# Kernel optimization log

Hardware: AMD Instinct MI355X
Metric: run time of the kernel (lower is better)

The kernel has to match this reference:

```python
import jax, jax.numpy as jnp
import numpy as np
from jax import lax

DISCOUNT = 0.99
NORMALIZE = True
EPS = 1e-9


def setup_inputs() -> dict:
    key = jax.random.key(0)
    k1, k2 = jax.random.split(key)
    B, T = 4096, 8192
    rewards = jax.random.normal(k1, (B, T), dtype=jnp.float32)
    done_flags = (jax.random.uniform(k2, (B, T)) < 0.01).astype(jnp.float32)
    return {"rewards": rewards, "done_flags": done_flags}


def _episode_returns(rewards, done_flags):
    # reverse-time recurrence: r_t = rew_t + gamma * r_{t+1} * (1 - done_t)
    rw = jnp.moveaxis(rewards, -1, 0)      # [T, B]
    dn = jnp.moveaxis(done_flags, -1, 0)   # [T, B]

    def step(carry, xs):
        r, d = xs
        ret = r + DISCOUNT * carry * (1.0 - d)
        return ret, ret

    # init carry = 0 makes the last step reduce to returns[-1] = rewards[-1]
    _, rets = lax.scan(step, jnp.zeros_like(rw[0]), (rw, dn), reverse=True)
    returns = jnp.moveaxis(rets, 0, -1)    # [B, T]

    if NORMALIZE:
        # torch: (returns - returns.mean()) / (returns.std(dim=-1) + 1e-9)
        # global mean, per-trajectory std (unbiased, matching torch default)
        std = jnp.std(returns, axis=-1, ddof=1, keepdims=True)
        returns = (returns - jnp.mean(returns)) / (std + EPS)
    return returns


def reference(rewards, done_flags):
    return _episode_returns(rewards, done_flags)
```

## Files before the change

kernel.cpp:

```cpp
#include <hip/hip_runtime.h>
#include <math.h>

#define TLEN   8192
#define BROWS  4096
#define NT     256
#define WPB    (NT / 64)
#define GRID   (BROWS / WPB)
#define TPW    256
#define NTW    (TLEN / TPW)
#define GAMMA  0.99f
#define EPSN   1e-9

typedef float f4 __attribute__((ext_vector_type(4)));

__device__ __forceinline__ void scan_tile4(const f4 r, const f4 d,
                                           const int lane, float& tc,
                                           float* __restrict__ dst,
                                           double& accS, double& accQ) {
  float rv[4], cv[4];
  rv[0] = r.x; rv[1] = r.y; rv[2] = r.z; rv[3] = r.w;
  cv[0] = fmaf(-GAMMA, d.x, GAMMA);
  cv[1] = fmaf(-GAMMA, d.y, GAMMA);
  cv[2] = fmaf(-GAMMA, d.z, GAMMA);
  cv[3] = fmaf(-GAMMA, d.w, GAMMA);

  float A = 0.f, P = 1.f;
#pragma unroll
  for (int j = 3; j >= 0; --j) {
    A = fmaf(cv[j], A, rv[j]);
    P *= cv[j];
    rv[j] = A;
    cv[j] = P;
  }

  float sA = A, sP = P;
#pragma unroll
  for (int dd = 1; dd < 64; dd <<= 1) {
    const float tA = __shfl_down(sA, dd);
    const float tP = __shfl_down(sP, dd);
    if (lane + dd < 64) { sA = fmaf(sP, tA, sA); sP *= tP; }
  }

  float eA = __shfl_down(sA, 1);
  float eP = __shfl_down(sP, 1);
  if (lane == 63) { eA = 0.f; eP = 1.f; }
  const float carry = fmaf(eP, tc, eA);

  const float gA = __shfl(sA, 0);
  const float gP = __shfl(sP, 0);
  tc = fmaf(gP, tc, gA);

  float fs = 0.f, fq = 0.f;
  f4 o;
  {
    const float r0 = fmaf(cv[0], carry, rv[0]);
    const float r1 = fmaf(cv[1], carry, rv[1]);
    const float r2 = fmaf(cv[2], carry, rv[2]);
    const float r3 = fmaf(cv[3], carry, rv[3]);
    o.x = r0; o.y = r1; o.z = r2; o.w = r3;
    fs = (r0 + r1) + (r2 + r3);
    fq = fmaf(r0, r0, fmaf(r1, r1, fmaf(r2, r2, r3 * r3)));
  }
  ((f4*)dst)[lane] = o;
  accS += (double)fs;
  accQ += (double)fq;
}

__global__ __launch_bounds__(NT, 4) void er_scan(const float* __restrict__ rew,
                                                 const float* __restrict__ don,
                                                 float* __restrict__ out,
                                                 double* __restrict__ rowSum,
                                                 float* __restrict__ rowInv) {
  const int tid  = threadIdx.x;
  const int lane = tid & 63;
  const int wv   = tid >> 6;
  const int row  = blockIdx.x * WPB + wv;
  const size_t rbase = (size_t)row * TLEN;

  const f4* gr = (const f4*)(rew + rbase);
  const f4* gd = (const f4*)(don + rbase);
  float* ob = out + rbase;

  f4 bR0, bR1, bR2, bR3, bD0, bD1, bD2, bD3;

  bR3 = gr[31 * 64 + lane]; bD3 = gd[31 * 64 + lane];
  bR2 = gr[30 * 64 + lane]; bD2 = gd[30 * 64 + lane];

  double accS = 0.0, accQ = 0.0;
  float  tc = 0.f;

#pragma unroll
  for (int kb = 31; kb >= 3; kb -= 4) {
    if (kb - 2 >= 0) { bR1 = gr[(kb - 2) * 64 + lane]; bD1 = gd[(kb - 2) * 64 + lane]; }
    __builtin_amdgcn_sched_barrier(0);
    scan_tile4(bR3, bD3, lane, tc, ob + (size_t)kb * TPW, accS, accQ);

    if (kb - 3 >= 0) { bR0 = gr[(kb - 3) * 64 + lane]; bD0 = gd[(kb - 3) * 64 + lane]; }
    __builtin_amdgcn_sched_barrier(0);
    scan_tile4(bR2, bD2, lane, tc, ob + (size_t)(kb - 1) * TPW, accS, accQ);

    if (kb - 4 >= 0) { bR3 = gr[(kb - 4) * 64 + lane]; bD3 = gd[(kb - 4) * 64 + lane]; }
    __builtin_amdgcn_sched_barrier(0);
    scan_tile4(bR1, bD1, lane, tc, ob + (size_t)(kb - 2) * TPW, accS, accQ);

    if (kb - 5 >= 0) { bR2 = gr[(kb - 5) * 64 + lane]; bD2 = gd[(kb - 5) * 64 + lane]; }
    __builtin_amdgcn_sched_barrier(0);
    scan_tile4(bR0, bD0, lane, tc, ob + (size_t)(kb - 3) * TPW, accS, accQ);
  }

  double ds = accS, dq = accQ;
#pragma unroll
  for (int d = 32; d >= 1; d >>= 1) {
    ds += __shfl_down(ds, d);
    dq += __shfl_down(dq, d);
  }
  if (lane == 0) {
    rowSum[row] = ds;
    double var = (dq - ds * ds / (double)TLEN) / (double)(TLEN - 1);
    if (var < 0.0) var = 0.0;
    rowInv[row] = (float)(1.0 / (sqrt(var) + EPSN));
  }
}

__global__ __launch_bounds__(256) void er_mean(const double* __restrict__ rowSum,
                                               float* __restrict__ meanPtr) {
  const int tid = threadIdx.x;
  double s = 0.0;
  for (int i = tid; i < BROWS; i += 256) s += rowSum[i];
#pragma unroll
  for (int d = 32; d >= 1; d >>= 1) s += __shfl_down(s, d);
  __shared__ double red[4];
  const int lane = tid & 63, wv = tid >> 6;
  if (lane == 0) red[wv] = s;
  __syncthreads();
  if (tid == 0) {
    const double t = red[0] + red[1] + red[2] + red[3];
    *meanPtr = (float)(t / ((double)BROWS * (double)TLEN));
  }
}

__global__ __launch_bounds__(256) void er_norm(float* __restrict__ out,
                                               const float* __restrict__ rowInv,
                                               const float* __restrict__ meanPtr) {
  const int row = blockIdx.x;
  const float mean = *meanPtr;
  const float inv  = rowInv[row];
  f4* o4 = (f4*)(out + (size_t)row * TLEN);
#pragma unroll
  for (int i = threadIdx.x; i < TLEN / 4; i += 256) {
    f4 v = o4[i];
    v.x = (v.x - mean) * inv;
    v.y = (v.y - mean) * inv;
    v.z = (v.z - mean) * inv;
    v.w = (v.w - mean) * inv;
    o4[i] = v;
  }
}

extern "C" void kernel_launch(void* const* d_in, const int* in_sizes, int n_in,
                              void* d_out, int out_size, void* d_ws, size_t ws_size,
                              hipStream_t stream) {
  const float* rew = (const float*)d_in[0];
  const float* don = (const float*)d_in[1];
  float* out = (float*)d_out;

  double* rowSum  = (double*)d_ws;
  float*  rowInv  = (float*)((char*)d_ws + BROWS * 8);
  float*  meanPtr = (float*)((char*)d_ws + BROWS * 8 + BROWS * 4);

  er_scan<<<GRID, NT, 0, stream>>>(rew, don, out, rowSum, rowInv);
  er_mean<<<1, 256, 0, stream>>>(rowSum, meanPtr);
  er_norm<<<BROWS, 256, 0, stream>>>(out, rowInv, meanPtr);
}
```

Measured before the change: 352.1 us.

## Process 16 elements per lane per wave-scan tile to cut shuffle passes

```diff
diff --git a/kernel.cpp b/kernel.cpp
--- a/kernel.cpp
+++ b/kernel.cpp
@@ -6,27 +6,32 @@
 #define NT     256
 #define WPB    (NT / 64)
 #define GRID   (BROWS / WPB)
-#define TPW    256
+#define TPW    1024
 #define NTW    (TLEN / TPW)
+#define SEG    16
 #define GAMMA  0.99f
 #define EPSN   1e-9
 
 typedef float f4 __attribute__((ext_vector_type(4)));
 
-__device__ __forceinline__ void scan_tile4(const f4 r, const f4 d,
-                                           const int lane, float& tc,
-                                           float* __restrict__ dst,
-                                           double& accS, double& accQ) {
-  float rv[4], cv[4];
-  rv[0] = r.x; rv[1] = r.y; rv[2] = r.z; rv[3] = r.w;
-  cv[0] = fmaf(-GAMMA, d.x, GAMMA);
-  cv[1] = fmaf(-GAMMA, d.y, GAMMA);
-  cv[2] = fmaf(-GAMMA, d.z, GAMMA);
-  cv[3] = fmaf(-GAMMA, d.w, GAMMA);
+__device__ __forceinline__ void scan_tile16(const f4* R, const f4* D,
+                                            const int lane, float& tc,
+                                            float* __restrict__ dst,
+                                            double& accS, double& accQ) {
+  float rv[SEG], cv[SEG];
+#pragma unroll
+  for (int q = 0; q < 4; ++q) {
+    rv[4 * q + 0] = R[q].x; rv[4 * q + 1] = R[q].y;
+    rv[4 * q + 2] = R[q].z; rv[4 * q + 3] = R[q].w;
+    cv[4 * q + 0] = fmaf(-GAMMA, D[q].x, GAMMA);
+    cv[4 * q + 1] = fmaf(-GAMMA, D[q].y, GAMMA);
+    cv[4 * q + 2] = fmaf(-GAMMA, D[q].z, GAMMA);
+    cv[4 * q + 3] = fmaf(-GAMMA, D[q].w, GAMMA);
+  }
 
   float A = 0.f, P = 1.f;
 #pragma unroll
-  for (int j = 3; j >= 0; --j) {
+  for (int j = SEG - 1; j >= 0; --j) {
     A = fmaf(cv[j], A, rv[j]);
     P *= cv[j];
     rv[j] = A;
@@ -51,17 +56,18 @@
   tc = fmaf(gP, tc, gA);
 
   float fs = 0.f, fq = 0.f;
-  f4 o;
-  {
-    const float r0 = fmaf(cv[0], carry, rv[0]);
-    const float r1 = fmaf(cv[1], carry, rv[1]);
-    const float r2 = fmaf(cv[2], carry, rv[2]);
-    const float r3 = fmaf(cv[3], carry, rv[3]);
-    o.x = r0; o.y = r1; o.z = r2; o.w = r3;
-    fs = (r0 + r1) + (r2 + r3);
-    fq = fmaf(r0, r0, fmaf(r1, r1, fmaf(r2, r2, r3 * r3)));
+  f4* go = (f4*)dst + 4 * lane;
+#pragma unroll
+  for (int q = 0; q < 4; ++q) {
+    const float r0 = fmaf(cv[4 * q + 0], carry, rv[4 * q + 0]);
+    const float r1 = fmaf(cv[4 * q + 1], carry, rv[4 * q + 1]);
+    const float r2 = fmaf(cv[4 * q + 2], carry, rv[4 * q + 2]);
+    const float r3 = fmaf(cv[4 * q + 3], carry, rv[4 * q + 3]);
+    f4 o; o.x = r0; o.y = r1; o.z = r2; o.w = r3;
+    go[q] = o;
+    fs += (r0 + r1) + (r2 + r3);
+    fq = fmaf(r0, r0, fmaf(r1, r1, fmaf(r2, r2, fmaf(r3, r3, fq))));
   }
-  ((f4*)dst)[lane] = o;
   accS += (double)fs;
   accQ += (double)fq;
 }
@@ -81,31 +87,34 @@
   const f4* gd = (const f4*)(don + rbase);
   float* ob = out + rbase;
 
-  f4 bR0, bR1, bR2, bR3, bD0, bD1, bD2, bD3;
+  f4 aR[4], aD[4], bR[4], bD[4];
 
-  bR3 = gr[31 * 64 + lane]; bD3 = gd[31 * 64 + lane];
-  bR2 = gr[30 * 64 + lane]; bD2 = gd[30 * 64 + lane];
+  {
+    const int f = (NTW - 1) * (TPW / 4) + 4 * lane;
+#pragma unroll
+    for (int q = 0; q < 4; ++q) { aR[q] = gr[f + q]; aD[q] = gd[f + q]; }
+  }
 
   double accS = 0.0, accQ = 0.0;
   float  tc = 0.f;
 
 #pragma unroll
-  for (int kb = 31; kb >= 3; kb -= 4) {
-    if (kb - 2 >= 0) { bR1 = gr[(kb - 2) * 64 + lane]; bD1 = gd[(kb - 2) * 64 + lane]; }
+  for (int kb = NTW - 1; kb >= 1; kb -= 2) {
+    {
+      const int f = (kb - 1) * (TPW / 4) + 4 * lane;
+#pragma unroll
+      for (int q = 0; q < 4; ++q) { bR[q] = gr[f + q]; bD[q] = gd[f + q]; }
+    }
     __builtin_amdgcn_sched_barrier(0);
-    scan_tile4(bR3, bD3, lane, tc, ob + (size_t)kb * TPW, accS, accQ);
+    scan_tile16(aR, aD, lane, tc, ob + (size_t)kb * TPW, accS, accQ);
 
-    if (kb - 3 >= 0) { bR0 = gr[(kb - 3) * 64 + lane]; bD0 = gd[(kb - 3) * 64 + lane]; }
+    if (kb - 2 >= 0) {
+      const int f = (kb - 2) * (TPW / 4) + 4 * lane;
+#pragma unroll
+      for (int q = 0; q < 4; ++q) { aR[q] = gr[f + q]; aD[q] = gd[f + q]; }
+    }
     __builtin_amdgcn_sched_barrier(0);
-    scan_tile4(bR2, bD2, lane, tc, ob + (size_t)(kb - 1) * TPW, accS, accQ);
-
-    if (kb - 4 >= 0) { bR3 = gr[(kb - 4) * 64 + lane]; bD3 = gd[(kb - 4) * 64 + lane]; }
-    __builtin_amdgcn_sched_barrier(0);
-    scan_tile4(bR1, bD1, lane, tc, ob + (size_t)(kb - 2) * TPW, accS, accQ);
-
-    if (kb - 5 >= 0) { bR2 = gr[(kb - 5) * 64 + lane]; bD2 = gd[(kb - 5) * 64 + lane]; }
-    __builtin_amdgcn_sched_barrier(0);
-    scan_tile4(bR0, bD0, lane, tc, ob + (size_t)(kb - 3) * TPW, accS, accQ);
+    scan_tile16(bR, bD, lane, tc, ob + (size_t)(kb - 1) * TPW, accS, accQ);
   }
 
   double ds = accS, dq = accQ;
```

New measurement: 357.6 us. No clear change (+1.6%).
